# Performance work log

Measured on AMD Instinct MI355X. Metric: run time of the kernel, lower is better.

## Reference

```python
import jax, jax.numpy as jnp
from jax import lax
import numpy as np

L, B, T, H, OUT = 2, 32, 1024, 512, 512


def setup_inputs() -> dict:
    key = jax.random.key(0)
    ks = jax.random.split(key, 8)
    stdv = 1.0 / np.sqrt(H)
    u = lambda k, shape: jax.random.uniform(k, shape, jnp.float32, -stdv, stdv)
    return {
        "x": jax.random.normal(ks[0], (B, T, H), jnp.float32),
        "h0": jnp.zeros((L, B, H), jnp.float32),
        "W_ih": u(ks[1], (L, 3 * H, H)),
        "b_ih": u(ks[2], (L, 3 * H)),
        "W_hh": u(ks[3], (L, 3 * H, H)),
        "b_hh": u(ks[4], (L, 3 * H)),
        "fc_W": u(ks[5], (OUT, H)),
        "fc_b": u(ks[6], (OUT,)),
    }


def _gru_cell(x_t, h, W_ih_l, b_ih_l, W_hh_l, b_hh_l):
    # x_t: [B, in], h: [B, H]
    g_x = x_t @ W_ih_l.T + b_ih_l  # [B, 3H]
    g_h = h @ W_hh_l.T + b_hh_l    # [B, 3H]
    xr, xu, xn = jnp.split(g_x, 3, axis=1)
    hr, hu, hn = jnp.split(g_h, 3, axis=1)
    r = jax.nn.sigmoid(xr + hr)
    u = jax.nn.sigmoid(xu + hu)
    n = jnp.tanh(xn + r * hn)
    return u * h + (1.0 - u) * n


def reference(x, h0, W_ih, b_ih, W_hh, b_hh, fc_W, fc_b):
    num_layers = W_ih.shape[0]

    def step(h, x_t):
        # h: [L, B, H], x_t: [B, H]
        inp = x_t
        new_h = []
        for l in range(num_layers):
            hy = _gru_cell(inp, h[l], W_ih[l], b_ih[l], W_hh[l], b_hh[l])
            new_h.append(hy)
            inp = hy
        return jnp.stack(new_h), None

    h_final, _ = lax.scan(step, h0, jnp.swapaxes(x, 0, 1))  # scan over time
    # torch module applies fc only to the last timestep's top-layer hidden
    return h_final[-1] @ fc_W.T + fc_b  # [B, OUT]
```

## Files before the change

kernel.cpp:

```cpp
#include <hip/hip_runtime.h>
#include <hip/hip_bf16.h>


typedef _Float16 f16x8 __attribute__((ext_vector_type(8)));
typedef float f32x4 __attribute__((ext_vector_type(4)));
typedef unsigned short u16;
typedef unsigned int u32;
typedef u32 u32x2 __attribute__((ext_vector_type(2)));

#define MFMA16(a,b,c) __builtin_amdgcn_mfma_f32_16x16x32_f16((a),(b),(c),0,0,0)
#define SB0 __builtin_amdgcn_sched_barrier(0)

static constexpr int B = 32, T = 1024, H = 512, G3 = 1536;

static constexpr size_t OFF_GX0   = 0;
static constexpr size_t OFF_H0ALL = OFF_GX0   + (size_t)T*B*G3*2;
static constexpr size_t OFF_H1ALL = OFF_H0ALL + (size_t)T*B*H*2;
static constexpr size_t OFF_WIH0  = OFF_H1ALL + (size_t)T*B*H*2;
static constexpr size_t OFF_H0I   = OFF_WIH0  + (size_t)G3*H*2;
static constexpr size_t OFF_H1I   = OFF_H0I   + (size_t)B*H*2;
static constexpr size_t OFF_H1F   = OFF_H1I   + (size_t)B*H*2;
static constexpr size_t OFF_FLG   = OFF_H1F   + (size_t)B*H*4;

__device__ __forceinline__ u16 f2h(float x){ _Float16 h=(_Float16)x; return __builtin_bit_cast(u16,h); }
__device__ __forceinline__ float h2f(u16 u){ _Float16 h=__builtin_bit_cast(_Float16,u); return (float)h; }

__device__ __forceinline__ u32 coh_load_u32(const u32* p){
  u32 r;
  asm volatile("global_load_dword %0, %1, off sc0 sc1\n\ts_waitcnt vmcnt(0)"
               : "=v"(r) : "v"(p) : "memory");
  return r;
}
__device__ __forceinline__ f16x8 coh_load16(const u16* p){
  f16x8 r;
  asm volatile("global_load_dwordx4 %0, %1, off sc0 sc1" : "=v"(r) : "v"(p));
  return r;
}
__device__ __forceinline__ void coh_store_u16(u16* p, u32 v){
  asm volatile("global_store_short %0, %1, off sc0 sc1" :: "v"(p), "v"(v) : "memory");
}
__device__ __forceinline__ void coh_store_u32(u32* p, u32 v){
  asm volatile("global_store_dword %0, %1, off sc0 sc1" :: "v"(p), "v"(v) : "memory");
}
#define VMWAIT8 asm volatile("s_waitcnt vmcnt(8)" ::: "memory")
#define VMWAIT0 asm volatile("s_waitcnt vmcnt(0)" ::: "memory")

__device__ __forceinline__ void poll64(const u32* base, u32 want, int lane){
  const u32* p = base + lane;
  while (!__all(coh_load_u32(p) == want)) {}
}

__device__ __forceinline__ float fsig(float x){ return 1.f/(1.f+__expf(-x)); }
__device__ __forceinline__ float ftanh(float x){
  x = fminf(15.f, fmaxf(-15.f, x));
  float e = __expf(-2.f*x);
  return (1.f-e)/(1.f+e);
}

__device__ __forceinline__ f16x8 lds_frag(const u16* wlds, int lrbase, int l15, int lk, int kk){
  int lr = lrbase + l15;
  int byte = lr*1024 + (((((kk<<5)+(lk<<3))<<1)) ^ ((lr&7)<<4));
  return *(const f16x8*)((const char*)wlds + byte);
}

__device__ __forceinline__ float gxval(u32x2 g, int j){
  u32 w = (j & 2) ? g[1] : g[0];
  return h2f((u16)(w >> ((j & 1) * 16)));
}

__global__ __launch_bounds__(256) void k0_prep(const float* __restrict__ wih,
                                               const float* __restrict__ h0in,
                                               u16* __restrict__ wih0f16,
                                               u16* __restrict__ h0i,
                                               u16* __restrict__ h1i,
                                               u32* __restrict__ flags){
  int i = blockIdx.x*256 + threadIdx.x;
  for (int idx=i; idx < G3*H; idx += 65536) wih0f16[idx] = f2h(wih[idx]);
  flags[i] = 0; flags[i + 65536] = 0;
  if (i < B*H){ h0i[i] = f2h(h0in[i]); h1i[i] = f2h(h0in[B*H + i]); }
}

__global__ __launch_bounds__(256) void k1_gx(const float* __restrict__ x,
                                             const u16* __restrict__ wih0,
                                             const float* __restrict__ bih0,
                                             u16* __restrict__ gxT){
  int t  = blockIdx.x / 6, nb = blockIdx.x % 6;
  int wave = threadIdx.x >> 6, lane = threadIdx.x & 63;
  int l15 = lane & 15, lk = lane >> 4;
  int colbase = nb*256 + wave*64;
  f32x4 acc[2][4] = {};
#pragma unroll 4
  for (int kk=0; kk<16; kk++){
    int k0 = kk*32 + lk*8;
    f16x8 a[2];
#pragma unroll
    for (int bm=0; bm<2; bm++){
      const f32x4* xp = (const f32x4*)(x + ((size_t)(bm*16+l15)*T + t)*H + k0);
      f32x4 x0 = xp[0], x1 = xp[1];
      f16x8 v;
#pragma unroll
      for (int q=0;q<4;q++){ v[q] = (_Float16)x0[q]; v[4+q] = (_Float16)x1[q]; }
      a[bm] = v;
    }
#pragma unroll
    for (int nt=0; nt<4; nt++){
      int col = colbase + nt*16 + l15;
      f16x8 bf = *(const f16x8*)(wih0 + (size_t)col*H + k0);
      acc[0][nt] = MFMA16(a[0], bf, acc[0][nt]);
      acc[1][nt] = MFMA16(a[1], bf, acc[1][nt]);
    }
  }
#pragma unroll
  for (int nt=0; nt<4; nt++){
    int col = colbase + nt*16 + l15;
    float bias = bih0[col];
#pragma unroll
    for (int bm=0; bm<2; bm++){
      u32 lo = (u32)f2h(acc[bm][nt][0]+bias) | ((u32)f2h(acc[bm][nt][1]+bias) << 16);
      u32 hi = (u32)f2h(acc[bm][nt][2]+bias) | ((u32)f2h(acc[bm][nt][3]+bias) << 16);
      u32x2 v; v[0] = lo; v[1] = hi;
      *(u32x2*)(gxT + ((size_t)t*G3 + col)*B + bm*16 + lk*4) = v;
    }
  }
}

__global__ __launch_bounds__(256,1) void k2_recur(const float* __restrict__ h0in,
                                                  const float* __restrict__ Wih,
                                                  const float* __restrict__ bih,
                                                  const float* __restrict__ Whh,
                                                  const float* __restrict__ bhh,
                                                  const u16* __restrict__ gxT,
                                                  u16* __restrict__ h0all,
                                                  u16* __restrict__ h1all,
                                                  const u16* __restrict__ h0i,
                                                  const u16* __restrict__ h1i,
                                                  float* __restrict__ h1fin,
                                                  u32* __restrict__ flags){
  __shared__ u16 wlds[96*512];
  const int wg  = blockIdx.x;
  const int tid = threadIdx.x;
  const bool isA = (wg < 16);
  u32* canA = flags;
  u32* canB = flags + (size_t)64*1024;

  {
    const int u0 = isA ? wg*32 : (wg-16)*16;
    for (int idx = tid; idx < 96*64; idx += 256){
      int lr = idx >> 6, k8 = idx & 63;
      const float* src;
      if (isA){
        int gate = lr >> 5, ul = lr & 31;
        src = Whh + ((size_t)(gate*512 + u0 + ul))*H + k8*8;
      } else if (lr < 48){
        int gate = lr >> 4, ul = lr & 15;
        src = Wih + (size_t)G3*H + ((size_t)(gate*512 + u0 + ul))*H + k8*8;
      } else {
        int lr2 = lr - 48; int gate = lr2 >> 4, ul = lr2 & 15;
        src = Whh + (size_t)G3*H + ((size_t)(gate*512 + u0 + ul))*H + k8*8;
      }
      f16x8 v;
#pragma unroll
      for (int q=0;q<8;q++) v[q] = (_Float16)src[q];
      *(f16x8*)((char*)wlds + lr*1024 + ((k8*16) ^ ((lr&7)<<4))) = v;
    }
  }
  __syncthreads();

  const int wave = tid >> 6, lane = tid & 63;
  const int l15 = lane & 15, lk = lane >> 4;

  if (isA){
    const int u0  = wg*32;
    const int bm  = wave >> 1, ntg = wave & 1;
    const int cu  = u0 + ntg*16 + l15;
    const int waveid = wg*4 + wave;
    const float bhr = bhh[cu], bhu = bhh[512+cu], bhn = bhh[1024+cu];
    float hown[4];
#pragma unroll
    for (int j=0;j<4;j++) hown[j] = h0in[(size_t)(bm*16 + lk*4 + j)*H + cu];

    for (int t=0; t<T; t++){
      const u16* gp = gxT + ((size_t)t*G3 + cu)*B + bm*16 + lk*4;
      u32x2 g0 = *(const u32x2*)gp;
      u32x2 g1 = *(const u32x2*)(gp + (size_t)512*B);
      u32x2 g2 = *(const u32x2*)(gp + (size_t)1024*B);

      if (t > 0) poll64(canA + (size_t)(t-1)*64, (u32)t, lane);
      const u16* hprev = (t==0) ? h0i : (h0all + (size_t)(t-1)*(B*H));
      const u16* hrow  = hprev + (size_t)(bm*16 + l15)*H + lk*8;

      f16x8 af[16];
#pragma unroll
      for (int kk=0; kk<16; kk++) af[kk] = coh_load16(hrow + kk*32);
      VMWAIT8; SB0;
      f32x4 aR{}, aU{}, aN{};
#pragma unroll
      for (int kk=0; kk<8; kk++){
        aR = MFMA16(af[kk], lds_frag(wlds,      ntg*16, l15, lk, kk), aR);
        aU = MFMA16(af[kk], lds_frag(wlds, 32 + ntg*16, l15, lk, kk), aU);
        aN = MFMA16(af[kk], lds_frag(wlds, 64 + ntg*16, l15, lk, kk), aN);
      }
      VMWAIT0; SB0;
#pragma unroll
      for (int kk=8; kk<16; kk++){
        aR = MFMA16(af[kk], lds_frag(wlds,      ntg*16, l15, lk, kk), aR);
        aU = MFMA16(af[kk], lds_frag(wlds, 32 + ntg*16, l15, lk, kk), aU);
        aN = MFMA16(af[kk], lds_frag(wlds, 64 + ntg*16, l15, lk, kk), aN);
      }
#pragma unroll
      for (int j=0;j<4;j++){
        float r = fsig(gxval(g0,j) + aR[j] + bhr);
        float u = fsig(gxval(g1,j) + aU[j] + bhu);
        float n = ftanh(gxval(g2,j) + r*(aN[j] + bhn));
        hown[j] = u*hown[j] + (1.f-u)*n;
        coh_store_u16(h0all + (size_t)t*(B*H) + (size_t)(bm*16 + lk*4 + j)*H + cu,
                      (u32)f2h(hown[j]));
      }
      VMWAIT0;
      if (lane == 0) coh_store_u32(canA + (size_t)t*64 + waveid, (u32)(t+1));
    }
  } else {
    if (wave >= 2) return;
    const int wg2 = wg - 16;
    const int u0 = wg2*16;
    const int bm = wave;
    const int cu = u0 + l15;
    const int waveid = wg2*2 + wave;
    const float br  = bih[G3 + cu]        + bhh[G3 + cu];
    const float bu  = bih[G3 + 512 + cu]  + bhh[G3 + 512 + cu];
    const float bni = bih[G3 + 1024 + cu];
    const float bnh = bhh[G3 + 1024 + cu];
    float hown[4];
#pragma unroll
    for (int j=0;j<4;j++) hown[j] = h0in[(size_t)B*H + (size_t)(bm*16 + lk*4 + j)*H + cu];

    for (int t=0; t<T; t++){
      poll64(canA + (size_t)t*64, (u32)(t+1), lane);
      const u16* xrow = h0all + (size_t)t*(B*H) + (size_t)(bm*16 + l15)*H + lk*8;
      f16x8 ax[16];
#pragma unroll
      for (int kk=0; kk<16; kk++) ax[kk] = coh_load16(xrow + kk*32);
      VMWAIT8; SB0;
      f32x4 xR{}, xU{}, xN{};
#pragma unroll
      for (int kk=0; kk<8; kk++){
        xR = MFMA16(ax[kk], lds_frag(wlds,  0, l15, lk, kk), xR);
        xU = MFMA16(ax[kk], lds_frag(wlds, 16, l15, lk, kk), xU);
        xN = MFMA16(ax[kk], lds_frag(wlds, 32, l15, lk, kk), xN);
      }
      VMWAIT0; SB0;
#pragma unroll
      for (int kk=8; kk<16; kk++){
        xR = MFMA16(ax[kk], lds_frag(wlds,  0, l15, lk, kk), xR);
        xU = MFMA16(ax[kk], lds_frag(wlds, 16, l15, lk, kk), xU);
        xN = MFMA16(ax[kk], lds_frag(wlds, 32, l15, lk, kk), xN);
      }

      if (t > 0) poll64(canB + (size_t)(t-1)*64, (u32)t, lane);
      const u16* hsrc = (t==0) ? h1i : (h1all + (size_t)(t-1)*(B*H));
      const u16* hrow = hsrc + (size_t)(bm*16 + l15)*H + lk*8;
      f16x8 ah[16];
#pragma unroll
      for (int kk=0; kk<16; kk++) ah[kk] = coh_load16(hrow + kk*32);
      VMWAIT8; SB0;
      f32x4 hR{}, hU{}, hN{};
#pragma unroll
      for (int kk=0; kk<8; kk++){
        hR = MFMA16(ah[kk], lds_frag(wlds, 48, l15, lk, kk), hR);
        hU = MFMA16(ah[kk], lds_frag(wlds, 64, l15, lk, kk), hU);
        hN = MFMA16(ah[kk], lds_frag(wlds, 80, l15, lk, kk), hN);
      }
      VMWAIT0; SB0;
#pragma unroll
      for (int kk=8; kk<16; kk++){
        hR = MFMA16(ah[kk], lds_frag(wlds, 48, l15, lk, kk), hR);
        hU = MFMA16(ah[kk], lds_frag(wlds, 64, l15, lk, kk), hU);
        hN = MFMA16(ah[kk], lds_frag(wlds, 80, l15, lk, kk), hN);
      }
#pragma unroll
      for (int j=0;j<4;j++){
        float r = fsig(xR[j] + hR[j] + br);
        float u = fsig(xU[j] + hU[j] + bu);
        float n = ftanh(xN[j] + bni + r*(hN[j] + bnh));
        hown[j] = u*hown[j] + (1.f-u)*n;
        int b = bm*16 + lk*4 + j;
        coh_store_u16(h1all + (size_t)t*(B*H) + (size_t)b*H + cu, (u32)f2h(hown[j]));
        if (t == T-1) h1fin[(size_t)b*H + cu] = hown[j];
      }
      VMWAIT0;
      if (lane == 0) coh_store_u32(canB + (size_t)t*64 + waveid, (u32)(t+1));
    }
  }
}

__global__ __launch_bounds__(256) void k3_fc(const float* __restrict__ h1fin,
                                             const float* __restrict__ fcW,
                                             const float* __restrict__ fcb,
                                             float* __restrict__ out){
  int g = blockIdx.x*256 + threadIdx.x;
  int b = g >> 9, o = g & 511;
  const f32x4* w = (const f32x4*)(fcW + (size_t)o*H);
  const f32x4* h = (const f32x4*)(h1fin + (size_t)b*H);
  float acc = fcb[o];
#pragma unroll 4
  for (int k=0;k<128;k++){
    f32x4 wv = w[k], hv = h[k];
    acc += wv[0]*hv[0] + wv[1]*hv[1] + wv[2]*hv[2] + wv[3]*hv[3];
  }
  out[g] = acc;
}

extern "C" void kernel_launch(void* const* d_in, const int* in_sizes, int n_in,
                              void* d_out, int out_size, void* d_ws, size_t ws_size,
                              hipStream_t stream) {
  const float* x    = (const float*)d_in[0];
  const float* h0   = (const float*)d_in[1];
  const float* Wih  = (const float*)d_in[2];
  const float* bihv = (const float*)d_in[3];
  const float* Whh  = (const float*)d_in[4];
  const float* bhhv = (const float*)d_in[5];
  const float* fcW  = (const float*)d_in[6];
  const float* fcb  = (const float*)d_in[7];
  float* out = (float*)d_out;

  char* ws = (char*)d_ws;
  u16* gxT     = (u16*)(ws + OFF_GX0);
  u16* h0all   = (u16*)(ws + OFF_H0ALL);
  u16* h1all   = (u16*)(ws + OFF_H1ALL);
  u16* wih0f16 = (u16*)(ws + OFF_WIH0);
  u16* h0i     = (u16*)(ws + OFF_H0I);
  u16* h1i     = (u16*)(ws + OFF_H1I);
  float* h1fin = (float*)(ws + OFF_H1F);
  u32* flags   = (u32*)(ws + OFF_FLG);

  k0_prep<<<256, 256, 0, stream>>>(Wih, h0, wih0f16, h0i, h1i, flags);
  k1_gx<<<T*6, 256, 0, stream>>>(x, wih0f16, bihv, gxT);
  k2_recur<<<48, 256, 0, stream>>>(h0, Wih, bihv, Whh, bhhv,
                                   gxT, h0all, h1all, h0i, h1i, h1fin, flags);
  k3_fc<<<64, 256, 0, stream>>>(h1fin, fcW, fcb, out);
}
```

Before: 6.382 ms.

## Tag hidden states with timestep, keep weights in registers, split layer-1 waves

Hidden-state elements are now stored as 32-bit words whose high half carries the timestep tag. Readers validate the tags after loading and retry on mismatch, so producers no longer wait on store completion before raising flags. Recurrent weights move from LDS into per-wave VGPRs. Layer-1 work is split so two waves compute the input projection and two compute the hidden projection concurrently, exchanging partial sums through LDS. Layer-1 hidden history becomes an 8-slot ring and the next step's gx is prefetched. In exchange, h0 traffic doubles, k0 must zero a larger region, and register pressure rises sharply.

```diff
diff --git a/kernel.cpp b/kernel.cpp
--- a/kernel.cpp
+++ b/kernel.cpp
@@ -7,20 +7,24 @@
 typedef unsigned short u16;
 typedef unsigned int u32;
 typedef u32 u32x2 __attribute__((ext_vector_type(2)));
+typedef u32 u32x4 __attribute__((ext_vector_type(4)));
 
 #define MFMA16(a,b,c) __builtin_amdgcn_mfma_f32_16x16x32_f16((a),(b),(c),0,0,0)
 #define SB0 __builtin_amdgcn_sched_barrier(0)
+#define PERM_LO 0x05040100u
+#define PERM_HI 0x07060302u
 
 static constexpr int B = 32, T = 1024, H = 512, G3 = 1536;
 
-static constexpr size_t OFF_GX0   = 0;
-static constexpr size_t OFF_H0ALL = OFF_GX0   + (size_t)T*B*G3*2;
-static constexpr size_t OFF_H1ALL = OFF_H0ALL + (size_t)T*B*H*2;
-static constexpr size_t OFF_WIH0  = OFF_H1ALL + (size_t)T*B*H*2;
-static constexpr size_t OFF_H0I   = OFF_WIH0  + (size_t)G3*H*2;
-static constexpr size_t OFF_H1I   = OFF_H0I   + (size_t)B*H*2;
-static constexpr size_t OFF_H1F   = OFF_H1I   + (size_t)B*H*2;
-static constexpr size_t OFF_FLG   = OFF_H1F   + (size_t)B*H*4;
+static constexpr size_t OFF_GX0    = 0;
+static constexpr size_t OFF_H0ALL  = OFF_GX0   + (size_t)T*B*G3*2;
+static constexpr size_t OFF_H1RING = OFF_H0ALL + (size_t)T*B*H*4;
+static constexpr size_t OFF_CAN    = OFF_H1RING + (size_t)8*B*H*4;
+static constexpr size_t OFF_WIH0   = OFF_CAN   + (size_t)2*1024*64*4;
+static constexpr size_t OFF_H0I    = OFF_WIH0  + (size_t)G3*H*2;
+static constexpr size_t OFF_H1I    = OFF_H0I   + (size_t)B*H*2;
+static constexpr size_t OFF_H1F    = OFF_H1I   + (size_t)B*H*2;
+static constexpr size_t ZERO_BYTES = OFF_WIH0 - OFF_H0ALL;
 
 __device__ __forceinline__ u16 f2h(float x){ _Float16 h=(_Float16)x; return __builtin_bit_cast(u16,h); }
 __device__ __forceinline__ float h2f(u16 u){ _Float16 h=__builtin_bit_cast(_Float16,u); return (float)h; }
@@ -31,23 +35,71 @@
                : "=v"(r) : "v"(p) : "memory");
   return r;
 }
-__device__ __forceinline__ f16x8 coh_load16(const u16* p){
-  f16x8 r;
+__device__ __forceinline__ u32x4 coh_load_x4(const u32* p){
+  u32x4 r;
   asm volatile("global_load_dwordx4 %0, %1, off sc0 sc1" : "=v"(r) : "v"(p));
   return r;
 }
-__device__ __forceinline__ void coh_store_u16(u16* p, u32 v){
-  asm volatile("global_store_short %0, %1, off sc0 sc1" :: "v"(p), "v"(v) : "memory");
-}
 __device__ __forceinline__ void coh_store_u32(u32* p, u32 v){
   asm volatile("global_store_dword %0, %1, off sc0 sc1" :: "v"(p), "v"(v) : "memory");
 }
-#define VMWAIT8 asm volatile("s_waitcnt vmcnt(8)" ::: "memory")
 #define VMWAIT0 asm volatile("s_waitcnt vmcnt(0)" ::: "memory")
 
 __device__ __forceinline__ void poll64(const u32* base, u32 want, int lane){
   const u32* p = base + lane;
   while (!__all(coh_load_u32(p) == want)) {}
+}
+
+__device__ __forceinline__ void tag_load16(f16x8* af, const u32* hp, u32 ww){
+  for (;;){
+    u32x4 q[32];
+#pragma unroll
+    for (int kk=0; kk<16; kk++){
+      q[2*kk]   = coh_load_x4(hp + kk*32);
+      q[2*kk+1] = coh_load_x4(hp + kk*32 + 4);
+    }
+    VMWAIT0; SB0;
+    u32 diff = 0;
+#pragma unroll
+    for (int kk=0; kk<16; kk++){
+      u32x4 a = q[2*kk], b = q[2*kk+1];
+      diff |= (__builtin_amdgcn_perm(a[1],a[0],PERM_HI) ^ ww);
+      diff |= (__builtin_amdgcn_perm(a[3],a[2],PERM_HI) ^ ww);
+      diff |= (__builtin_amdgcn_perm(b[1],b[0],PERM_HI) ^ ww);
+      diff |= (__builtin_amdgcn_perm(b[3],b[2],PERM_HI) ^ ww);
+      u32x4 v;
+      v[0] = __builtin_amdgcn_perm(a[1],a[0],PERM_LO);
+      v[1] = __builtin_amdgcn_perm(a[3],a[2],PERM_LO);
+      v[2] = __builtin_amdgcn_perm(b[1],b[0],PERM_LO);
+      v[3] = __builtin_amdgcn_perm(b[3],b[2],PERM_LO);
+      af[kk] = __builtin_bit_cast(f16x8, v);
+    }
+    if (__all(diff == 0)) break;
+  }
+}
+
+__device__ __forceinline__ void load_wf(f16x8 (*wf)[16], const float* Wbase, int cu, int lk){
+#pragma unroll
+  for (int g=0; g<3; g++)
+#pragma unroll
+    for (int kk=0; kk<16; kk++){
+      const float* s = Wbase + ((size_t)(g*512 + cu))*H + kk*32 + lk*8;
+      f32x4 s0 = *(const f32x4*)s, s1 = *(const f32x4*)(s+4);
+      f16x8 v;
+#pragma unroll
+      for (int e=0; e<4; e++){ v[e] = (_Float16)s0[e]; v[4+e] = (_Float16)s1[e]; }
+      wf[g][kk] = v;
+    }
+}
+
+__device__ __forceinline__ void mm48(f32x4& R, f32x4& U, f32x4& N,
+                                     const f16x8* af, const f16x8 (*wf)[16]){
+#pragma unroll
+  for (int kk=0; kk<16; kk++){
+    R = MFMA16(af[kk], wf[0][kk], R);
+    U = MFMA16(af[kk], wf[1][kk], U);
+    N = MFMA16(af[kk], wf[2][kk], N);
+  }
 }
 
 __device__ __forceinline__ float fsig(float x){ return 1.f/(1.f+__expf(-x)); }
@@ -56,13 +108,6 @@
   float e = __expf(-2.f*x);
   return (1.f-e)/(1.f+e);
 }
-
-__device__ __forceinline__ f16x8 lds_frag(const u16* wlds, int lrbase, int l15, int lk, int kk){
-  int lr = lrbase + l15;
-  int byte = lr*1024 + (((((kk<<5)+(lk<<3))<<1)) ^ ((lr&7)<<4));
-  return *(const f16x8*)((const char*)wlds + byte);
-}
-
 __device__ __forceinline__ float gxval(u32x2 g, int j){
   u32 w = (j & 2) ? g[1] : g[0];
   return h2f((u16)(w >> ((j & 1) * 16)));
@@ -73,10 +118,12 @@
                                                u16* __restrict__ wih0f16,
                                                u16* __restrict__ h0i,
                                                u16* __restrict__ h1i,
-                                               u32* __restrict__ flags){
+                                               u32x4* __restrict__ zbase){
   int i = blockIdx.x*256 + threadIdx.x;
-  for (int idx=i; idx < G3*H; idx += 65536) wih0f16[idx] = f2h(wih[idx]);
-  flags[i] = 0; flags[i + 65536] = 0;
+  const int NZ = (int)(ZERO_BYTES / 16);
+  u32x4 z; z[0]=0; z[1]=0; z[2]=0; z[3]=0;
+  for (int idx=i; idx < NZ; idx += 131072) zbase[idx] = z;
+  for (int idx=i; idx < G3*H; idx += 131072) wih0f16[idx] = f2h(wih[idx]);
   if (i < B*H){ h0i[i] = f2h(h0in[i]); h1i[i] = f2h(h0in[B*H + i]); }
 }
 
@@ -130,165 +177,138 @@
                                                   const float* __restrict__ Whh,
                                                   const float* __restrict__ bhh,
                                                   const u16* __restrict__ gxT,
-                                                  u16* __restrict__ h0all,
-                                                  u16* __restrict__ h1all,
+                                                  u32* __restrict__ h0u,
+                                                  u32* __restrict__ h1r,
                                                   const u16* __restrict__ h0i,
                                                   const u16* __restrict__ h1i,
                                                   float* __restrict__ h1fin,
-                                                  u32* __restrict__ flags){
-  __shared__ u16 wlds[96*512];
+                                                  u32* __restrict__ can){
+  __shared__ __align__(16) float part[2][2][64][12];
   const int wg  = blockIdx.x;
   const int tid = threadIdx.x;
-  const bool isA = (wg < 16);
-  u32* canA = flags;
-  u32* canB = flags + (size_t)64*1024;
-
-  {
-    const int u0 = isA ? wg*32 : (wg-16)*16;
-    for (int idx = tid; idx < 96*64; idx += 256){
-      int lr = idx >> 6, k8 = idx & 63;
-      const float* src;
-      if (isA){
-        int gate = lr >> 5, ul = lr & 31;
-        src = Whh + ((size_t)(gate*512 + u0 + ul))*H + k8*8;
-      } else if (lr < 48){
-        int gate = lr >> 4, ul = lr & 15;
-        src = Wih + (size_t)G3*H + ((size_t)(gate*512 + u0 + ul))*H + k8*8;
-      } else {
-        int lr2 = lr - 48; int gate = lr2 >> 4, ul = lr2 & 15;
-        src = Whh + (size_t)G3*H + ((size_t)(gate*512 + u0 + ul))*H + k8*8;
-      }
-      f16x8 v;
-#pragma unroll
-      for (int q=0;q<8;q++) v[q] = (_Float16)src[q];
-      *(f16x8*)((char*)wlds + lr*1024 + ((k8*16) ^ ((lr&7)<<4))) = v;
-    }
-  }
-  __syncthreads();
-
   const int wave = tid >> 6, lane = tid & 63;
   const int l15 = lane & 15, lk = lane >> 4;
-
-  if (isA){
+  u32* canA = can;
+  u32* canB = can + (size_t)64*1024;
+
+  if (wg < 16){
     const int u0  = wg*32;
     const int bm  = wave >> 1, ntg = wave & 1;
     const int cu  = u0 + ntg*16 + l15;
     const int waveid = wg*4 + wave;
+    f16x8 wf[3][16];
+    load_wf(wf, Whh, cu, lk);
     const float bhr = bhh[cu], bhu = bhh[512+cu], bhn = bhh[1024+cu];
     float hown[4];
 #pragma unroll
     for (int j=0;j<4;j++) hown[j] = h0in[(size_t)(bm*16 + lk*4 + j)*H + cu];
 
+    u32x2 g0, g1, g2;
+    {
+      const u16* gp = gxT + ((size_t)0*G3 + cu)*B + bm*16 + lk*4;
+      g0 = *(const u32x2*)gp;
+      g1 = *(const u32x2*)(gp + (size_t)512*B);
+      g2 = *(const u32x2*)(gp + (size_t)1024*B);
+    }
+
     for (int t=0; t<T; t++){
-      const u16* gp = gxT + ((size_t)t*G3 + cu)*B + bm*16 + lk*4;
-      u32x2 g0 = *(const u32x2*)gp;
-      u32x2 g1 = *(const u32x2*)(gp + (size_t)512*B);
-      u32x2 g2 = *(const u32x2*)(gp + (size_t)1024*B);
-
-      if (t > 0) poll64(canA + (size_t)(t-1)*64, (u32)t, lane);
-      const u16* hprev = (t==0) ? h0i : (h0all + (size_t)(t-1)*(B*H));
-      const u16* hrow  = hprev + (size_t)(bm*16 + l15)*H + lk*8;
-
       f16x8 af[16];
-#pragma unroll
-      for (int kk=0; kk<16; kk++) af[kk] = coh_load16(hrow + kk*32);
-      VMWAIT8; SB0;
+      if (t == 0){
+        const u16* hr = h0i + (size_t)(bm*16 + l15)*H + lk*8;
+#pragma unroll
+        for (int kk=0; kk<16; kk++) af[kk] = *(const f16x8*)(hr + kk*32);
+      } else {
+        poll64(canA + (size_t)(t-1)*64, (u32)t, lane);
+        const u32* hp = h0u + ((size_t)(t-1)*B + bm*16 + l15)*H + lk*8;
+        tag_load16(af, hp, (u32)t * 0x10001u);
+      }
+      int tn = (t+1 < T) ? (t+1) : t;
+      const u16* gp = gxT + ((size_t)tn*G3 + cu)*B + bm*16 + lk*4;
+      u32x2 ng0 = *(const u32x2*)gp;
+      u32x2 ng1 = *(const u32x2*)(gp + (size_t)512*B);
+      u32x2 ng2 = *(const u32x2*)(gp + (size_t)1024*B);
+
       f32x4 aR{}, aU{}, aN{};
-#pragma unroll
-      for (int kk=0; kk<8; kk++){
-        aR = MFMA16(af[kk], lds_frag(wlds,      ntg*16, l15, lk, kk), aR);
-        aU = MFMA16(af[kk], lds_frag(wlds, 32 + ntg*16, l15, lk, kk), aU);
-        aN = MFMA16(af[kk], lds_frag(wlds, 64 + ntg*16, l15, lk, kk), aN);
-      }
-      VMWAIT0; SB0;
-#pragma unroll
-      for (int kk=8; kk<16; kk++){
-        aR = MFMA16(af[kk], lds_frag(wlds,      ntg*16, l15, lk, kk), aR);
-        aU = MFMA16(af[kk], lds_frag(wlds, 32 + ntg*16, l15, lk, kk), aU);
-        aN = MFMA16(af[kk], lds_frag(wlds, 64 + ntg*16, l15, lk, kk), aN);
-      }
+      mm48(aR, aU, aN, af, wf);
+
+      const u32 tago = ((u32)(t+1)) << 16;
 #pragma unroll
       for (int j=0;j<4;j++){
         float r = fsig(gxval(g0,j) + aR[j] + bhr);
         float u = fsig(gxval(g1,j) + aU[j] + bhu);
         float n = ftanh(gxval(g2,j) + r*(aN[j] + bhn));
         hown[j] = u*hown[j] + (1.f-u)*n;
-        coh_store_u16(h0all + (size_t)t*(B*H) + (size_t)(bm*16 + lk*4 + j)*H + cu,
-                      (u32)f2h(hown[j]));
+        int b = bm*16 + lk*4 + j;
+        coh_store_u32(h0u + ((size_t)t*B + b)*H + cu, (u32)f2h(hown[j]) | tago);
       }
-      VMWAIT0;
       if (lane == 0) coh_store_u32(canA + (size_t)t*64 + waveid, (u32)(t+1));
+      g0 = ng0; g1 = ng1; g2 = ng2;
     }
   } else {
-    if (wave >= 2) return;
     const int wg2 = wg - 16;
-    const int u0 = wg2*16;
-    const int bm = wave;
-    const int cu = u0 + l15;
-    const int waveid = wg2*2 + wave;
-    const float br  = bih[G3 + cu]        + bhh[G3 + cu];
-    const float bu  = bih[G3 + 512 + cu]  + bhh[G3 + 512 + cu];
-    const float bni = bih[G3 + 1024 + cu];
-    const float bnh = bhh[G3 + 1024 + cu];
-    float hown[4];
-#pragma unroll
-    for (int j=0;j<4;j++) hown[j] = h0in[(size_t)B*H + (size_t)(bm*16 + lk*4 + j)*H + cu];
-
-    for (int t=0; t<T; t++){
-      poll64(canA + (size_t)t*64, (u32)(t+1), lane);
-      const u16* xrow = h0all + (size_t)t*(B*H) + (size_t)(bm*16 + l15)*H + lk*8;
-      f16x8 ax[16];
-#pragma unroll
-      for (int kk=0; kk<16; kk++) ax[kk] = coh_load16(xrow + kk*32);
-      VMWAIT8; SB0;
-      f32x4 xR{}, xU{}, xN{};
-#pragma unroll
-      for (int kk=0; kk<8; kk++){
-        xR = MFMA16(ax[kk], lds_frag(wlds,  0, l15, lk, kk), xR);
-        xU = MFMA16(ax[kk], lds_frag(wlds, 16, l15, lk, kk), xU);
-        xN = MFMA16(ax[kk], lds_frag(wlds, 32, l15, lk, kk), xN);
+    const int u0  = wg2*16;
+    const int cu  = u0 + l15;
+    const bool isX = (wave < 2);
+    const int bm  = isX ? wave : (wave - 2);
+
+    if (isX){
+      f16x8 wf[3][16];
+      load_wf(wf, Wih + (size_t)G3*H, cu, lk);
+      for (int t=0; t<T; t++){
+        poll64(canA + (size_t)t*64, (u32)(t+1), lane);
+        f16x8 ax[16];
+        const u32* hp = h0u + ((size_t)t*B + bm*16 + l15)*H + lk*8;
+        tag_load16(ax, hp, (u32)(t+1) * 0x10001u);
+        f32x4 xR{}, xU{}, xN{};
+        mm48(xR, xU, xN, ax, wf);
+        float* pp = &part[t&1][bm][lane][0];
+        *(f32x4*)(pp+0) = xR; *(f32x4*)(pp+4) = xU; *(f32x4*)(pp+8) = xN;
+        __syncthreads();
       }
-      VMWAIT0; SB0;
-#pragma unroll
-      for (int kk=8; kk<16; kk++){
-        xR = MFMA16(ax[kk], lds_frag(wlds,  0, l15, lk, kk), xR);
-        xU = MFMA16(ax[kk], lds_frag(wlds, 16, l15, lk, kk), xU);
-        xN = MFMA16(ax[kk], lds_frag(wlds, 32, l15, lk, kk), xN);
+    } else {
+      f16x8 wf[3][16];
+      load_wf(wf, Whh + (size_t)G3*H, cu, lk);
+      const int waveid = wg2*2 + bm;
+      const float br  = bih[G3 + cu]        + bhh[G3 + cu];
+      const float bu  = bih[G3 + 512 + cu]  + bhh[G3 + 512 + cu];
+      const float bni = bih[G3 + 1024 + cu];
+      const float bnh = bhh[G3 + 1024 + cu];
+      float hown[4];
+#pragma unroll
+      for (int j=0;j<4;j++) hown[j] = h0in[(size_t)B*H + (size_t)(bm*16 + lk*4 + j)*H + cu];
+
+      for (int t=0; t<T; t++){
+        f16x8 ah[16];
+        if (t == 0){
+          const u16* hr = h1i + (size_t)(bm*16 + l15)*H + lk*8;
+#pragma unroll
+          for (int kk=0; kk<16; kk++) ah[kk] = *(const f16x8*)(hr + kk*32);
+        } else {
+          poll64(canB + (size_t)(t-1)*64, (u32)t, lane);
+          const u32* hp = h1r + ((size_t)((t-1)&7)*B + bm*16 + l15)*H + lk*8;
+          tag_load16(ah, hp, (u32)t * 0x10001u);
+        }
+        f32x4 hR{}, hU{}, hN{};
+        mm48(hR, hU, hN, ah, wf);
+        __syncthreads();
+        const float* pp = &part[t&1][bm][lane][0];
+        f32x4 xR = *(const f32x4*)(pp+0);
+        f32x4 xU = *(const f32x4*)(pp+4);
+        f32x4 xN = *(const f32x4*)(pp+8);
+
+        const u32 tago = ((u32)(t+1)) << 16;
+#pragma unroll
+        for (int j=0;j<4;j++){
+          float r = fsig(xR[j] + hR[j] + br);
+          float u = fsig(xU[j] + hU[j] + bu);
+          float n = ftanh(xN[j] + bni + r*(hN[j] + bnh));
+          hown[j] = u*hown[j] + (1.f-u)*n;
+          int b = bm*16 + lk*4 + j;
+          coh_store_u32(h1r + ((size_t)(t&7)*B + b)*H + cu, (u32)f2h(hown[j]) | tago);
+          if (t == T-1) h1fin[(size_t)b*H + cu] = hown[j];
+        }
+        if (lane == 0) coh_store_u32(canB + (size_t)t*64 + waveid, (u32)(t+1));
       }
-
-      if (t > 0) poll64(canB + (size_t)(t-1)*64, (u32)t, lane);
-      const u16* hsrc = (t==0) ? h1i : (h1all + (size_t)(t-1)*(B*H));
-      const u16* hrow = hsrc + (size_t)(bm*16 + l15)*H + lk*8;
-      f16x8 ah[16];
-#pragma unroll
-      for (int kk=0; kk<16; kk++) ah[kk] = coh_load16(hrow + kk*32);
-      VMWAIT8; SB0;
-      f32x4 hR{}, hU{}, hN{};
-#pragma unroll
-      for (int kk=0; kk<8; kk++){
-        hR = MFMA16(ah[kk], lds_frag(wlds, 48, l15, lk, kk), hR);
-        hU = MFMA16(ah[kk], lds_frag(wlds, 64, l15, lk, kk), hU);
-        hN = MFMA16(ah[kk], lds_frag(wlds, 80, l15, lk, kk), hN);
-      }
-      VMWAIT0; SB0;
-#pragma unroll
-      for (int kk=8; kk<16; kk++){
-        hR = MFMA16(ah[kk], lds_frag(wlds, 48, l15, lk, kk), hR);
-        hU = MFMA16(ah[kk], lds_frag(wlds, 64, l15, lk, kk), hU);
-        hN = MFMA16(ah[kk], lds_frag(wlds, 80, l15, lk, kk), hN);
-      }
-#pragma unroll
-      for (int j=0;j<4;j++){
-        float r = fsig(xR[j] + hR[j] + br);
-        float u = fsig(xU[j] + hU[j] + bu);
-        float n = ftanh(xN[j] + bni + r*(hN[j] + bnh));
-        hown[j] = u*hown[j] + (1.f-u)*n;
-        int b = bm*16 + lk*4 + j;
-        coh_store_u16(h1all + (size_t)t*(B*H) + (size_t)b*H + cu, (u32)f2h(hown[j]));
-        if (t == T-1) h1fin[(size_t)b*H + cu] = hown[j];
-      }
-      VMWAIT0;
-      if (lane == 0) coh_store_u32(canB + (size_t)t*64 + waveid, (u32)(t+1));
     }
   }
 }
@@ -325,17 +345,17 @@
 
   char* ws = (char*)d_ws;
   u16* gxT     = (u16*)(ws + OFF_GX0);
-  u16* h0all   = (u16*)(ws + OFF_H0ALL);
-  u16* h1all   = (u16*)(ws + OFF_H1ALL);
+  u32* h0u     = (u32*)(ws + OFF_H0ALL);
+  u32* h1r     = (u32*)(ws + OFF_H1RING);
+  u32* can     = (u32*)(ws + OFF_CAN);
   u16* wih0f16 = (u16*)(ws + OFF_WIH0);
   u16* h0i     = (u16*)(ws + OFF_H0I);
   u16* h1i     = (u16*)(ws + OFF_H1I);
   float* h1fin = (float*)(ws + OFF_H1F);
-  u32* flags   = (u32*)(ws + OFF_FLG);
-
-  k0_prep<<<256, 256, 0, stream>>>(Wih, h0, wih0f16, h0i, h1i, flags);
+
+  k0_prep<<<512, 256, 0, stream>>>(Wih, h0, wih0f16, h0i, h1i, (u32x4*)(ws + OFF_H0ALL));
   k1_gx<<<T*6, 256, 0, stream>>>(x, wih0f16, bihv, gxT);
   k2_recur<<<48, 256, 0, stream>>>(h0, Wih, bihv, Whh, bhhv,
-                                   gxT, h0all, h1all, h0i, h1i, h1fin, flags);
+                                   gxT, h0u, h1r, h0i, h1i, h1fin, can);
   k3_fc<<<64, 256, 0, stream>>>(h1fin, fcW, fcb, out);
 }
```

Result: slower. 8.779 ms (+37.6%).

## Split layer-1 input and recurrent GEMMs across waves; keep layer-0 weights in registers

Applied to the files above, without the earlier changes.

Layer-0 workgroups now hold their W_hh slice as f16 fragments in registers instead of reading it from LDS on every step. Layer-1 workgroups previously ran only two of their four waves, each doing both the input-projection GEMM and the recurrent GEMM in sequence. Now waves 2-3 compute the input projection of the layer-0 output and hand it to waves 0-1 through a double-buffered LDS area with a block barrier. Waves 0-1 do only the recurrent GEMM and the gate math, which shortens layer 1's serial critical path per step. The cost is higher register pressure (48 fragment registers per lane) and a __syncthreads per step that couples the producer and consumer waves.

```diff
diff --git a/kernel.cpp b/kernel.cpp
--- a/kernel.cpp
+++ b/kernel.cpp
@@ -10,17 +10,20 @@
 
 #define MFMA16(a,b,c) __builtin_amdgcn_mfma_f32_16x16x32_f16((a),(b),(c),0,0,0)
 #define SB0 __builtin_amdgcn_sched_barrier(0)
+#define VMWAIT8 asm volatile("s_waitcnt vmcnt(8)" ::: "memory")
+#define VMWAIT0 asm volatile("s_waitcnt vmcnt(0)" ::: "memory")
 
 static constexpr int B = 32, T = 1024, H = 512, G3 = 1536;
 
-static constexpr size_t OFF_GX0   = 0;
-static constexpr size_t OFF_H0ALL = OFF_GX0   + (size_t)T*B*G3*2;
-static constexpr size_t OFF_H1ALL = OFF_H0ALL + (size_t)T*B*H*2;
-static constexpr size_t OFF_WIH0  = OFF_H1ALL + (size_t)T*B*H*2;
-static constexpr size_t OFF_H0I   = OFF_WIH0  + (size_t)G3*H*2;
-static constexpr size_t OFF_H1I   = OFF_H0I   + (size_t)B*H*2;
-static constexpr size_t OFF_H1F   = OFF_H1I   + (size_t)B*H*2;
-static constexpr size_t OFF_FLG   = OFF_H1F   + (size_t)B*H*4;
+static constexpr size_t OFF_GX  = 0;
+static constexpr size_t OFF_H0  = OFF_GX + (size_t)T*G3*B*2;
+static constexpr size_t OFF_H1  = OFF_H0 + (size_t)T*B*H*2;
+static constexpr size_t OFF_CA  = OFF_H1 + (size_t)T*B*H*2;
+static constexpr size_t OFF_CB  = OFF_CA + (size_t)T*64*4;
+static constexpr size_t OFF_W0  = OFF_CB + (size_t)T*64*4;
+static constexpr size_t OFF_H0I = OFF_W0 + (size_t)G3*H*2;
+static constexpr size_t OFF_H1I = OFF_H0I + (size_t)B*H*2;
+static constexpr size_t OFF_H1F = OFF_H1I + (size_t)B*H*2;
 
 __device__ __forceinline__ u16 f2h(float x){ _Float16 h=(_Float16)x; return __builtin_bit_cast(u16,h); }
 __device__ __forceinline__ float h2f(u16 u){ _Float16 h=__builtin_bit_cast(_Float16,u); return (float)h; }
@@ -42,8 +45,6 @@
 __device__ __forceinline__ void coh_store_u32(u32* p, u32 v){
   asm volatile("global_store_dword %0, %1, off sc0 sc1" :: "v"(p), "v"(v) : "memory");
 }
-#define VMWAIT8 asm volatile("s_waitcnt vmcnt(8)" ::: "memory")
-#define VMWAIT0 asm volatile("s_waitcnt vmcnt(0)" ::: "memory")
 
 __device__ __forceinline__ void poll64(const u32* base, u32 want, int lane){
   const u32* p = base + lane;
@@ -56,16 +57,28 @@
   float e = __expf(-2.f*x);
   return (1.f-e)/(1.f+e);
 }
-
+__device__ __forceinline__ float gxval(u32x2 g, int j){
+  u32 w = (j & 2) ? g[1] : g[0];
+  return h2f((u16)(w >> ((j & 1) * 16)));
+}
+
+__device__ __forceinline__ void load_wf(f16x8 (*wf)[16], const float* Wbase, int cu, int lk){
+#pragma unroll
+  for (int g=0; g<3; g++)
+#pragma unroll
+    for (int kk=0; kk<16; kk++){
+      const float* s = Wbase + ((size_t)(g*512 + cu))*H + kk*32 + lk*8;
+      f32x4 s0 = *(const f32x4*)s, s1 = *(const f32x4*)(s+4);
+      f16x8 v;
+#pragma unroll
+      for (int e=0; e<4; e++){ v[e]=(_Float16)s0[e]; v[4+e]=(_Float16)s1[e]; }
+      wf[g][kk] = v;
+    }
+}
 __device__ __forceinline__ f16x8 lds_frag(const u16* wlds, int lrbase, int l15, int lk, int kk){
   int lr = lrbase + l15;
   int byte = lr*1024 + (((((kk<<5)+(lk<<3))<<1)) ^ ((lr&7)<<4));
   return *(const f16x8*)((const char*)wlds + byte);
-}
-
-__device__ __forceinline__ float gxval(u32x2 g, int j){
-  u32 w = (j & 2) ? g[1] : g[0];
-  return h2f((u16)(w >> ((j & 1) * 16)));
 }
 
 __global__ __launch_bounds__(256) void k0_prep(const float* __restrict__ wih,
@@ -73,10 +86,10 @@
                                                u16* __restrict__ wih0f16,
                                                u16* __restrict__ h0i,
                                                u16* __restrict__ h1i,
-                                               u32* __restrict__ flags){
+                                               u32* __restrict__ cans){
   int i = blockIdx.x*256 + threadIdx.x;
-  for (int idx=i; idx < G3*H; idx += 65536) wih0f16[idx] = f2h(wih[idx]);
-  flags[i] = 0; flags[i + 65536] = 0;
+  for (int idx=i; idx<G3*H; idx+=65536) wih0f16[idx] = f2h(wih[idx]);
+  cans[i] = 0; cans[i + 65536] = 0;
   if (i < B*H){ h0i[i] = f2h(h0in[i]); h1i[i] = f2h(h0in[B*H + i]); }
 }
 
@@ -95,11 +108,11 @@
     f16x8 a[2];
 #pragma unroll
     for (int bm=0; bm<2; bm++){
-      const f32x4* xp = (const f32x4*)(x + ((size_t)(bm*16+l15)*T + t)*H + k0);
-      f32x4 x0 = xp[0], x1 = xp[1];
+      const f32x4* xp_ = (const f32x4*)(x + ((size_t)(bm*16+l15)*T + t)*H + k0);
+      f32x4 x0 = xp_[0], x1 = xp_[1];
       f16x8 v;
 #pragma unroll
-      for (int q=0;q<4;q++){ v[q] = (_Float16)x0[q]; v[4+q] = (_Float16)x1[q]; }
+      for (int q=0;q<4;q++){ v[q]=(_Float16)x0[q]; v[4+q]=(_Float16)x1[q]; }
       a[bm] = v;
     }
 #pragma unroll
@@ -118,62 +131,32 @@
     for (int bm=0; bm<2; bm++){
       u32 lo = (u32)f2h(acc[bm][nt][0]+bias) | ((u32)f2h(acc[bm][nt][1]+bias) << 16);
       u32 hi = (u32)f2h(acc[bm][nt][2]+bias) | ((u32)f2h(acc[bm][nt][3]+bias) << 16);
-      u32x2 v; v[0] = lo; v[1] = hi;
+      u32x2 v; v[0]=lo; v[1]=hi;
       *(u32x2*)(gxT + ((size_t)t*G3 + col)*B + bm*16 + lk*4) = v;
     }
   }
 }
 
 __global__ __launch_bounds__(256,1) void k2_recur(const float* __restrict__ h0in,
-                                                  const float* __restrict__ Wih,
-                                                  const float* __restrict__ bih,
-                                                  const float* __restrict__ Whh,
-                                                  const float* __restrict__ bhh,
-                                                  const u16* __restrict__ gxT,
-                                                  u16* __restrict__ h0all,
-                                                  u16* __restrict__ h1all,
-                                                  const u16* __restrict__ h0i,
-                                                  const u16* __restrict__ h1i,
-                                                  float* __restrict__ h1fin,
-                                                  u32* __restrict__ flags){
-  __shared__ u16 wlds[96*512];
-  const int wg  = blockIdx.x;
-  const int tid = threadIdx.x;
-  const bool isA = (wg < 16);
-  u32* canA = flags;
-  u32* canB = flags + (size_t)64*1024;
-
-  {
-    const int u0 = isA ? wg*32 : (wg-16)*16;
-    for (int idx = tid; idx < 96*64; idx += 256){
-      int lr = idx >> 6, k8 = idx & 63;
-      const float* src;
-      if (isA){
-        int gate = lr >> 5, ul = lr & 31;
-        src = Whh + ((size_t)(gate*512 + u0 + ul))*H + k8*8;
-      } else if (lr < 48){
-        int gate = lr >> 4, ul = lr & 15;
-        src = Wih + (size_t)G3*H + ((size_t)(gate*512 + u0 + ul))*H + k8*8;
-      } else {
-        int lr2 = lr - 48; int gate = lr2 >> 4, ul = lr2 & 15;
-        src = Whh + (size_t)G3*H + ((size_t)(gate*512 + u0 + ul))*H + k8*8;
-      }
-      f16x8 v;
-#pragma unroll
-      for (int q=0;q<8;q++) v[q] = (_Float16)src[q];
-      *(f16x8*)((char*)wlds + lr*1024 + ((k8*16) ^ ((lr&7)<<4))) = v;
-    }
-  }
-  __syncthreads();
-
+    const float* __restrict__ Wih, const float* __restrict__ bih,
+    const float* __restrict__ Whh, const float* __restrict__ bhh,
+    const u16* __restrict__ gxT,
+    u16* __restrict__ h0all, u16* __restrict__ h1all,
+    u32* __restrict__ canA, u32* __restrict__ canB,
+    const u16* __restrict__ h0i, const u16* __restrict__ h1i,
+    float* __restrict__ h1fin)
+{
+  __shared__ __align__(16) u16 wlds[96*512];
+  __shared__ __align__(16) float part[2][2][64][12];
+  const int wg = blockIdx.x, tid = threadIdx.x;
   const int wave = tid >> 6, lane = tid & 63;
   const int l15 = lane & 15, lk = lane >> 4;
 
-  if (isA){
-    const int u0  = wg*32;
-    const int bm  = wave >> 1, ntg = wave & 1;
-    const int cu  = u0 + ntg*16 + l15;
+  if (wg < 16){
+    const int bm = wave >> 1, ug = wave & 1;
+    const int cu = wg*32 + ug*16 + l15;
     const int waveid = wg*4 + wave;
+    f16x8 wf[3][16]; load_wf(wf, Whh, cu, lk);
     const float bhr = bhh[cu], bhu = bhh[512+cu], bhn = bhh[1024+cu];
     float hown[4];
 #pragma unroll
@@ -186,9 +169,8 @@
       u32x2 g2 = *(const u32x2*)(gp + (size_t)1024*B);
 
       if (t > 0) poll64(canA + (size_t)(t-1)*64, (u32)t, lane);
-      const u16* hprev = (t==0) ? h0i : (h0all + (size_t)(t-1)*(B*H));
-      const u16* hrow  = hprev + (size_t)(bm*16 + l15)*H + lk*8;
-
+      const u16* hrow = ((t==0) ? h0i : (h0all + (size_t)(t-1)*(B*H)))
+                        + (size_t)(bm*16 + l15)*H + lk*8;
       f16x8 af[16];
 #pragma unroll
       for (int kk=0; kk<16; kk++) af[kk] = coh_load16(hrow + kk*32);
@@ -196,16 +178,16 @@
       f32x4 aR{}, aU{}, aN{};
 #pragma unroll
       for (int kk=0; kk<8; kk++){
-        aR = MFMA16(af[kk], lds_frag(wlds,      ntg*16, l15, lk, kk), aR);
-        aU = MFMA16(af[kk], lds_frag(wlds, 32 + ntg*16, l15, lk, kk), aU);
-        aN = MFMA16(af[kk], lds_frag(wlds, 64 + ntg*16, l15, lk, kk), aN);
+        aR = MFMA16(af[kk], wf[0][kk], aR);
+        aU = MFMA16(af[kk], wf[1][kk], aU);
+        aN = MFMA16(af[kk], wf[2][kk], aN);
       }
       VMWAIT0; SB0;
 #pragma unroll
       for (int kk=8; kk<16; kk++){
-        aR = MFMA16(af[kk], lds_frag(wlds,      ntg*16, l15, lk, kk), aR);
-        aU = MFMA16(af[kk], lds_frag(wlds, 32 + ntg*16, l15, lk, kk), aU);
-        aN = MFMA16(af[kk], lds_frag(wlds, 64 + ntg*16, l15, lk, kk), aN);
+        aR = MFMA16(af[kk], wf[0][kk], aR);
+        aU = MFMA16(af[kk], wf[1][kk], aU);
+        aN = MFMA16(af[kk], wf[2][kk], aN);
       }
 #pragma unroll
       for (int j=0;j<4;j++){
@@ -220,75 +202,105 @@
       if (lane == 0) coh_store_u32(canA + (size_t)t*64 + waveid, (u32)(t+1));
     }
   } else {
-    if (wave >= 2) return;
     const int wg2 = wg - 16;
-    const int u0 = wg2*16;
-    const int bm = wave;
+    const int u0  = wg2*16;
+    for (int idx = tid; idx < 96*64; idx += 256){
+      int lr = idx >> 6, k8 = idx & 63;
+      const float* src;
+      if (lr < 48){
+        int gate = lr >> 4, ul = lr & 15;
+        src = Wih + (size_t)G3*H + ((size_t)(gate*512 + u0 + ul))*H + k8*8;
+      } else {
+        int lr2 = lr - 48; int gate = lr2 >> 4, ul = lr2 & 15;
+        src = Whh + (size_t)G3*H + ((size_t)(gate*512 + u0 + ul))*H + k8*8;
+      }
+      f16x8 v;
+#pragma unroll
+      for (int q=0;q<8;q++) v[q] = (_Float16)src[q];
+      *(f16x8*)((char*)wlds + lr*1024 + ((k8*16) ^ ((lr&7)<<4))) = v;
+    }
+    __syncthreads();
+
     const int cu = u0 + l15;
-    const int waveid = wg2*2 + wave;
-    const float br  = bih[G3 + cu]        + bhh[G3 + cu];
-    const float bu  = bih[G3 + 512 + cu]  + bhh[G3 + 512 + cu];
-    const float bni = bih[G3 + 1024 + cu];
-    const float bnh = bhh[G3 + 1024 + cu];
-    float hown[4];
-#pragma unroll
-    for (int j=0;j<4;j++) hown[j] = h0in[(size_t)B*H + (size_t)(bm*16 + lk*4 + j)*H + cu];
-
-    for (int t=0; t<T; t++){
-      poll64(canA + (size_t)t*64, (u32)(t+1), lane);
-      const u16* xrow = h0all + (size_t)t*(B*H) + (size_t)(bm*16 + l15)*H + lk*8;
-      f16x8 ax[16];
-#pragma unroll
-      for (int kk=0; kk<16; kk++) ax[kk] = coh_load16(xrow + kk*32);
-      VMWAIT8; SB0;
-      f32x4 xR{}, xU{}, xN{};
-#pragma unroll
-      for (int kk=0; kk<8; kk++){
-        xR = MFMA16(ax[kk], lds_frag(wlds,  0, l15, lk, kk), xR);
-        xU = MFMA16(ax[kk], lds_frag(wlds, 16, l15, lk, kk), xU);
-        xN = MFMA16(ax[kk], lds_frag(wlds, 32, l15, lk, kk), xN);
-      }
-      VMWAIT0; SB0;
-#pragma unroll
-      for (int kk=8; kk<16; kk++){
-        xR = MFMA16(ax[kk], lds_frag(wlds,  0, l15, lk, kk), xR);
-        xU = MFMA16(ax[kk], lds_frag(wlds, 16, l15, lk, kk), xU);
-        xN = MFMA16(ax[kk], lds_frag(wlds, 32, l15, lk, kk), xN);
-      }
-
-      if (t > 0) poll64(canB + (size_t)(t-1)*64, (u32)t, lane);
-      const u16* hsrc = (t==0) ? h1i : (h1all + (size_t)(t-1)*(B*H));
-      const u16* hrow = hsrc + (size_t)(bm*16 + l15)*H + lk*8;
-      f16x8 ah[16];
-#pragma unroll
-      for (int kk=0; kk<16; kk++) ah[kk] = coh_load16(hrow + kk*32);
-      VMWAIT8; SB0;
-      f32x4 hR{}, hU{}, hN{};
-#pragma unroll
-      for (int kk=0; kk<8; kk++){
-        hR = MFMA16(ah[kk], lds_frag(wlds, 48, l15, lk, kk), hR);
-        hU = MFMA16(ah[kk], lds_frag(wlds, 64, l15, lk, kk), hU);
-        hN = MFMA16(ah[kk], lds_frag(wlds, 80, l15, lk, kk), hN);
-      }
-      VMWAIT0; SB0;
-#pragma unroll
-      for (int kk=8; kk<16; kk++){
-        hR = MFMA16(ah[kk], lds_frag(wlds, 48, l15, lk, kk), hR);
-        hU = MFMA16(ah[kk], lds_frag(wlds, 64, l15, lk, kk), hU);
-        hN = MFMA16(ah[kk], lds_frag(wlds, 80, l15, lk, kk), hN);
-      }
-#pragma unroll
-      for (int j=0;j<4;j++){
-        float r = fsig(xR[j] + hR[j] + br);
-        float u = fsig(xU[j] + hU[j] + bu);
-        float n = ftanh(xN[j] + bni + r*(hN[j] + bnh));
-        hown[j] = u*hown[j] + (1.f-u)*n;
-        int b = bm*16 + lk*4 + j;
-        coh_store_u16(h1all + (size_t)t*(B*H) + (size_t)b*H + cu, (u32)f2h(hown[j]));
-        if (t == T-1) h1fin[(size_t)b*H + cu] = hown[j];
-      }
-      VMWAIT0;
-      if (lane == 0) coh_store_u32(canB + (size_t)t*64 + waveid, (u32)(t+1));
+
+    if (wave >= 2){
+      const int bm = wave - 2;
+      for (int t=0; t<T; t++){
+        poll64(canA + (size_t)t*64, (u32)(t+1), lane);
+        const u16* xrow = h0all + (size_t)t*(B*H) + (size_t)(bm*16 + l15)*H + lk*8;
+        f16x8 ax[16];
+#pragma unroll
+        for (int kk=0; kk<16; kk++) ax[kk] = coh_load16(xrow + kk*32);
+        VMWAIT8; SB0;
+        f32x4 xR{}, xU{}, xN{};
+#pragma unroll
+        for (int kk=0; kk<8; kk++){
+          xR = MFMA16(ax[kk], lds_frag(wlds,  0, l15, lk, kk), xR);
+          xU = MFMA16(ax[kk], lds_frag(wlds, 16, l15, lk, kk), xU);
+          xN = MFMA16(ax[kk], lds_frag(wlds, 32, l15, lk, kk), xN);
+        }
+        VMWAIT0; SB0;
+#pragma unroll
+        for (int kk=8; kk<16; kk++){
+          xR = MFMA16(ax[kk], lds_frag(wlds,  0, l15, lk, kk), xR);
+          xU = MFMA16(ax[kk], lds_frag(wlds, 16, l15, lk, kk), xU);
+          xN = MFMA16(ax[kk], lds_frag(wlds, 32, l15, lk, kk), xN);
+        }
+        float* pp = &part[t&1][bm][lane][0];
+        *(f32x4*)(pp+0) = xR; *(f32x4*)(pp+4) = xU; *(f32x4*)(pp+8) = xN;
+        __syncthreads();
+      }
+    } else {
+      const int bm = wave;
+      const int waveid = wg2*2 + bm;
+      const float br  = bih[G3 + cu]        + bhh[G3 + cu];
+      const float bu_ = bih[G3 + 512 + cu]  + bhh[G3 + 512 + cu];
+      const float bni = bih[G3 + 1024 + cu];
+      const float bnh = bhh[G3 + 1024 + cu];
+      float hown[4];
+#pragma unroll
+      for (int j=0;j<4;j++) hown[j] = h0in[(size_t)B*H + (size_t)(bm*16 + lk*4 + j)*H + cu];
+
+      for (int t=0; t<T; t++){
+        if (t > 0) poll64(canB + (size_t)(t-1)*64, (u32)t, lane);
+        const u16* hrow = ((t==0) ? h1i : (h1all + (size_t)(t-1)*(B*H)))
+                          + (size_t)(bm*16 + l15)*H + lk*8;
+        f16x8 ah[16];
+#pragma unroll
+        for (int kk=0; kk<16; kk++) ah[kk] = coh_load16(hrow + kk*32);
+        VMWAIT8; SB0;
+        f32x4 hR{}, hU{}, hN{};
+#pragma unroll
+        for (int kk=0; kk<8; kk++){
+          hR = MFMA16(ah[kk], lds_frag(wlds, 48, l15, lk, kk), hR);
+          hU = MFMA16(ah[kk], lds_frag(wlds, 64, l15, lk, kk), hU);
+          hN = MFMA16(ah[kk], lds_frag(wlds, 80, l15, lk, kk), hN);
+        }
+        VMWAIT0; SB0;
+#pragma unroll
+        for (int kk=8; kk<16; kk++){
+          hR = MFMA16(ah[kk], lds_frag(wlds, 48, l15, lk, kk), hR);
+          hU = MFMA16(ah[kk], lds_frag(wlds, 64, l15, lk, kk), hU);
+          hN = MFMA16(ah[kk], lds_frag(wlds, 80, l15, lk, kk), hN);
+        }
+        __syncthreads();
+        const float* pp = &part[t&1][bm][lane][0];
+        f32x4 xR = *(const f32x4*)(pp+0);
+        f32x4 xU = *(const f32x4*)(pp+4);
+        f32x4 xN = *(const f32x4*)(pp+8);
+#pragma unroll
+        for (int j=0;j<4;j++){
+          float r = fsig(xR[j] + hR[j] + br);
+          float u = fsig(xU[j] + hU[j] + bu_);
+          float n = ftanh(xN[j] + bni + r*(hN[j] + bnh));
+          hown[j] = u*hown[j] + (1.f-u)*n;
+          int b = bm*16 + lk*4 + j;
+          coh_store_u16(h1all + (size_t)t*(B*H) + (size_t)b*H + cu, (u32)f2h(hown[j]));
+          if (t == T-1) h1fin[(size_t)b*H + cu] = hown[j];
+        }
+        VMWAIT0;
+        if (lane == 0) coh_store_u32(canB + (size_t)t*64 + waveid, (u32)(t+1));
+      }
     }
   }
 }
@@ -324,18 +336,19 @@
   float* out = (float*)d_out;
 
   char* ws = (char*)d_ws;
-  u16* gxT     = (u16*)(ws + OFF_GX0);
-  u16* h0all   = (u16*)(ws + OFF_H0ALL);
-  u16* h1all   = (u16*)(ws + OFF_H1ALL);
-  u16* wih0f16 = (u16*)(ws + OFF_WIH0);
+  u16* gxT     = (u16*)(ws + OFF_GX);
+  u16* h0all   = (u16*)(ws + OFF_H0);
+  u16* h1all   = (u16*)(ws + OFF_H1);
+  u32* canA    = (u32*)(ws + OFF_CA);
+  u32* canB    = (u32*)(ws + OFF_CB);
+  u16* wih0f16 = (u16*)(ws + OFF_W0);
   u16* h0i     = (u16*)(ws + OFF_H0I);
   u16* h1i     = (u16*)(ws + OFF_H1I);
   float* h1fin = (float*)(ws + OFF_H1F);
-  u32* flags   = (u32*)(ws + OFF_FLG);
-
-  k0_prep<<<256, 256, 0, stream>>>(Wih, h0, wih0f16, h0i, h1i, flags);
+
+  k0_prep<<<256, 256, 0, stream>>>(Wih, h0, wih0f16, h0i, h1i, canA);
   k1_gx<<<T*6, 256, 0, stream>>>(x, wih0f16, bihv, gxT);
-  k2_recur<<<48, 256, 0, stream>>>(h0, Wih, bihv, Whh, bhhv,
-                                   gxT, h0all, h1all, h0i, h1i, h1fin, flags);
+  k2_recur<<<48, 256, 0, stream>>>(h0, Wih, bihv, Whh, bhhv, gxT,
+                                   h0all, h1all, canA, canB, h0i, h1i, h1fin);
   k3_fc<<<64, 256, 0, stream>>>(h1fin, fcW, fcb, out);
 }
```

Result: slower. 7.967 ms (+24.8%).
